# Kernel optimization log

Hardware: AMD Instinct MI355X
Metric: run time of the kernel (lower is better)

The kernel has to match this reference:

```python
import jax, jax.numpy as jnp
import numpy as np

B, T = 4, 16000
V = 256      # input_channels (token vocab)
R = 256      # residual_channels
S = 512      # skip_channels
O = 256      # output_channels
L = 16       # layers
DIL = 256    # 2 ** (floor(log2(max_dilation=128)) + 1) -- same for every layer (as in source)


def setup_inputs() -> dict:
    key = jax.random.key(0)
    ks = jax.random.split(key, 12)
    tokens = jax.random.randint(ks[0], (B, T), 0, V)
    embed = jax.random.normal(ks[1], (V, R), jnp.float32) * 0.05
    dilate_w = jax.random.normal(ks[2], (L, 2 * R, R, 2), jnp.float32) * 0.05
    dilate_b = jax.random.normal(ks[3], (L, 2 * R), jnp.float32) * 0.01
    res_w = jax.random.normal(ks[4], (L - 1, R, R), jnp.float32) * 0.05
    res_b = jax.random.normal(ks[5], (L - 1, R), jnp.float32) * 0.01
    skip_w = jax.random.normal(ks[6], (L, S, R), jnp.float32) * 0.05
    skip_b = jax.random.normal(ks[7], (L, S), jnp.float32) * 0.01
    conv_out_w = jax.random.normal(ks[8], (O, S), jnp.float32) * 0.05
    conv_end_w = jax.random.normal(ks[9], (O, O), jnp.float32) * 0.05
    return {
        'tokens': tokens, 'embed': embed,
        'dilate_w': dilate_w, 'dilate_b': dilate_b,
        'res_w': res_w, 'res_b': res_b,
        'skip_w': skip_w, 'skip_b': skip_b,
        'conv_out_w': conv_out_w, 'conv_end_w': conv_end_w,
    }


def _wavenet(tokens, embed, dilate_w, dilate_b, res_w, res_b, skip_w, skip_b,
             conv_out_w, conv_end_w):
    x = embed[tokens]                 # [B,T,R]
    x = jnp.transpose(x, (0, 2, 1))   # [B,R,T]
    skip = None
    for l in range(L):
        # causal dilated conv, kernel=2: y[t] = W0 @ x[t-DIL] + W1 @ x[t] + b
        x_shift = jnp.pad(x, ((0, 0), (0, 0), (DIL, 0)))[:, :, :T]
        in_act = (jnp.einsum('oi,bit->bot', dilate_w[l, :, :, 0], x_shift)
                  + jnp.einsum('oi,bit->bot', dilate_w[l, :, :, 1], x)
                  + dilate_b[l][None, :, None])      # [B,2R,T]
        g = in_act[:, :R, :]                          # source uses SAME slice for tanh & sigmoid
        act = jnp.tanh(g) * jax.nn.sigmoid(g)         # [B,R,T]
        if l < L - 1:
            res = jnp.einsum('oi,bit->bot', res_w[l], act) + res_b[l][None, :, None]
            x = res + x
        s = jnp.einsum('si,bit->bst', skip_w[l], act) + skip_b[l][None, :, None]
        skip = s if skip is None else skip + s
    out = jax.nn.relu(skip)
    out = jnp.einsum('os,bst->bot', conv_out_w, out)
    out = jax.nn.relu(out)
    out = jnp.einsum('po,bot->bpt', conv_end_w, out)
    return jax.nn.softmax(out, axis=1)                # softmax over channel dim


def reference(tokens, embed, dilate_w, dilate_b, res_w, res_b, skip_w, skip_b,
              conv_out_w, conv_end_w):
    return _wavenet(tokens, embed, dilate_w, dilate_b, res_w, res_b,
                    skip_w, skip_b, conv_out_w, conv_end_w)
```

## Files before the change

kernel.cpp:

```cpp
#include <hip/hip_runtime.h>
#include <hip/hip_fp16.h>

#define TLEN 16000
#define BC 2
#define XPROWS 16256

typedef _Float16 h16;
typedef __attribute__((ext_vector_type(8))) _Float16 half8;
typedef __attribute__((ext_vector_type(4))) _Float16 half4;
typedef __attribute__((ext_vector_type(4))) float f32x4;

__device__ __forceinline__ void gload16(const void* g, void* l) {
  __builtin_amdgcn_global_load_lds((const __attribute__((address_space(1))) void*)g,
                                   (__attribute__((address_space(3))) void*)l, 16, 0, 0);
}

__device__ __forceinline__ float gated_act(float g) {
  float gc = fmaxf(g, -30.0f);
  float e1 = __expf(-gc);
  float e2 = e1 * e1;
  return (1.0f - e2) / ((1.0f + e2) * (1.0f + e1));
}

__global__ __launch_bounds__(256) void prep_k(
    const float* __restrict__ dw, const float* __restrict__ rw,
    const float* __restrict__ sw, const float* __restrict__ cow,
    const float* __restrict__ cew, const float* __restrict__ sb,
    h16* __restrict__ w2h, h16* __restrict__ rsw, h16* __restrict__ couth,
    h16* __restrict__ cendh, float* __restrict__ sbias, h16* __restrict__ x16p)
{
  size_t u = (size_t)blockIdx.x * 256 + threadIdx.x;
  if (u < 2097152) {
    int l = (int)(u >> 17);
    int rem = (int)(u & 131071);
    int o = rem >> 9, k = rem & 511;
    float v = (k < 256) ? dw[(((size_t)l * 512 + o) * 256 + k) * 2]
                        : dw[(((size_t)l * 512 + o) * 256 + (k - 256)) * 2 + 1];
    w2h[u] = (h16)v;
    return;
  }
  u -= 2097152;
  if (u < 3145728) {
    int l = (int)(u / 196608);
    int r = (int)(u % 196608);
    int row = r >> 8, c = r & 255;
    float v;
    if (row < 256) v = (l < 15) ? rw[((size_t)l * 256 + row) * 256 + c] : 0.f;
    else           v = sw[((size_t)l * 512 + (row - 256)) * 256 + c];
    rsw[u] = (h16)v;
    return;
  }
  u -= 3145728;
  if (u < 131072) { couth[u] = (h16)cow[u]; return; }
  u -= 131072;
  if (u < 65536) { cendh[u] = (h16)cew[u]; return; }
  u -= 65536;
  if (u < 512) {
    float s = 0.f;
    for (int l = 0; l < 16; l++) s += sb[(size_t)l * 512 + u];
    sbias[u] = s;
    return;
  }
  u -= 512;
  if (u < 131072) {
    int b = (int)(u >> 16), off = (int)(u & 65535);
    x16p[(size_t)b * XPROWS * 256 + off] = (h16)0.f;
  }
}

__global__ __launch_bounds__(256) void embed_k(
    const int* __restrict__ tok, const float* __restrict__ emb,
    float* __restrict__ x, h16* __restrict__ x16p)
{
  const int b = blockIdx.y;
  const size_t i = (size_t)blockIdx.x * 256 + threadIdx.x;
  const int t = (int)(i >> 6);
  const int c4 = (int)(i & 63) * 4;
  const int tk = tok[(size_t)b * TLEN + t];
  f32x4 v = *(const f32x4*)(emb + (size_t)tk * 256 + c4);
  *(f32x4*)(x + ((size_t)b * TLEN + t) * 256 + c4) = v;
  half4 hv;
#pragma unroll
  for (int j = 0; j < 4; j++) hv[j] = (h16)v[j];
  *(half4*)(x16p + (size_t)b * XPROWS * 256 + (size_t)(t + 256) * 256 + c4) = hv;
}

__global__ __launch_bounds__(256) void skipinit_k(
    const float* __restrict__ sbias, float* __restrict__ skip)
{
  const int b = blockIdx.y;
  const size_t i = (size_t)blockIdx.x * 256 + threadIdx.x;
  const int t = (int)(i >> 7);
  const int s4 = (int)(i & 127) * 4;
  *(f32x4*)(skip + ((size_t)b * TLEN + t) * 512 + s4) = *(const f32x4*)(sbias + s4);
}

__global__ __launch_bounds__(256) void cvt_k(
    const float* __restrict__ skip, h16* __restrict__ sk16)
{
  const size_t i = ((size_t)blockIdx.y * 8192000) + ((size_t)blockIdx.x * 256 + threadIdx.x) * 4;
  f32x4 v = *(const f32x4*)(skip + i);
  half4 hv;
#pragma unroll
  for (int j = 0; j < 4; j++) hv[j] = (h16)fmaxf(v[j], 0.f);
  *(half4*)(sk16 + i) = hv;
}

template<int KTOT, int MODE>
__global__ __launch_bounds__(256) void gemm3_k(
    const h16* __restrict__ A, const h16* __restrict__ W,
    const float* __restrict__ bias, h16* __restrict__ o16,
    float* __restrict__ of32, float* __restrict__ ofskip, int nskip0)
{
  constexpr int NT = KTOT / 32;
  __shared__ h16 As[2][64 * 32];
  __shared__ h16 Bs[2][256 * 32];
  __shared__ h16 tbuf[4][16][72];

  const int tid  = threadIdx.x;
  const int lane = tid & 63;
  const int w    = tid >> 6;
  const int r16  = lane & 15;
  const int kg   = lane >> 4;
  const int t0   = blockIdx.x * 64;
  const int by   = blockIdx.y;
  const int bz   = blockIdx.z;
  const int srow  = lane >> 2;
  const int sunit = (lane & 3) * 8;

  const h16* Ab;
  if constexpr (MODE == 0)      Ab = A + (size_t)bz * XPROWS * 256;
  else if constexpr (MODE == 1) Ab = A + (size_t)bz * TLEN * 256;
  else                          Ab = A + (size_t)bz * TLEN * 512;
  const int n0w = (MODE == 1) ? by * 256 : 0;

  auto stage = [&](int bi, int kk) {
    const int k0 = kk * 32;
    {
      const h16* src;
      if constexpr (MODE == 0)
        src = Ab + (size_t)(t0 + w * 16 + srow + (k0 < 256 ? 0 : 256)) * 256 + (k0 & 255) + sunit;
      else if constexpr (MODE == 1)
        src = Ab + (size_t)(t0 + w * 16 + srow) * 256 + k0 + sunit;
      else
        src = Ab + (size_t)(t0 + w * 16 + srow) * 512 + k0 + sunit;
      gload16(src, &As[bi][(w * 16) * 32]);
    }
#pragma unroll
    for (int q = 0; q < 4; q++) {
      const h16* src = W + (size_t)(n0w + w * 64 + q * 16 + srow) * KTOT + k0 + sunit;
      gload16(src, &Bs[bi][(w * 64 + q * 16) * 32]);
    }
  };

  f32x4 acc[4][4];
#pragma unroll
  for (int i = 0; i < 4; i++)
#pragma unroll
    for (int j = 0; j < 4; j++) acc[i][j] = (f32x4){0.f, 0.f, 0.f, 0.f};

  stage(0, 0);
  __syncthreads();

  for (int t = 0; t < NT; t++) {
    const int cur = t & 1;
    if (t + 1 < NT) stage(cur ^ 1, t + 1);
    half8 af[4], bf[4];
#pragma unroll
    for (int mi = 0; mi < 4; mi++)
      af[mi] = *(const half8*)&As[cur][(mi * 16 + r16) * 32 + kg * 8];
#pragma unroll
    for (int ni = 0; ni < 4; ni++)
      bf[ni] = *(const half8*)&Bs[cur][(w * 64 + ni * 16 + r16) * 32 + kg * 8];
#pragma unroll
    for (int mi = 0; mi < 4; mi++)
#pragma unroll
      for (int ni = 0; ni < 4; ni++)
        acc[mi][ni] = __builtin_amdgcn_mfma_f32_16x16x32_f16(af[mi], bf[ni], acc[mi][ni], 0, 0, 0);
    __syncthreads();
  }

  const int rr = lane >> 2;
  const int cc = (lane & 3) * 16;
  const bool is_res = (MODE == 1) && (n0w < nskip0);

  if constexpr (MODE == 1) {
    if (!is_res) {
#pragma unroll
      for (int mi = 0; mi < 4; mi++)
#pragma unroll
        for (int ni = 0; ni < 4; ni++) {
          const int s = n0w + w * 64 + ni * 16 + r16 - nskip0;
#pragma unroll
          for (int g = 0; g < 4; g++) {
            const int t = t0 + mi * 16 + kg * 4 + g;
            const size_t ix = ((size_t)bz * TLEN + t) * 512 + s;
            ofskip[ix] += acc[mi][ni][g];
          }
        }
      return;
    }
  }

#pragma unroll
  for (int mi = 0; mi < 4; mi++) {
#pragma unroll
    for (int ni = 0; ni < 4; ni++) {
      const int nl = w * 64 + ni * 16 + r16;
#pragma unroll
      for (int g = 0; g < 4; g++) {
        float v = acc[mi][ni][g];
        const int t = t0 + mi * 16 + kg * 4 + g;
        if constexpr (MODE == 0) {
          v = gated_act(v + bias[nl]);
        } else if constexpr (MODE == 1) {
          const size_t ix = ((size_t)bz * TLEN + t) * 256 + nl;
          v = of32[ix] + v + bias[nl];
          of32[ix] = v;
        } else {
          v = fmaxf(v, 0.f);
        }
        tbuf[w][kg * 4 + g][ni * 16 + r16] = (h16)v;
      }
    }
    h16* dst;
    if constexpr (MODE == 1)
      dst = o16 + (size_t)bz * XPROWS * 256 + (size_t)(256 + t0 + mi * 16 + rr) * 256 + w * 64 + cc;
    else
      dst = o16 + ((size_t)bz * TLEN + t0 + mi * 16 + rr) * 256 + w * 64 + cc;
    *(half8*)dst       = *(const half8*)&tbuf[w][rr][cc];
    *(half8*)(dst + 8) = *(const half8*)&tbuf[w][rr][cc + 8];
  }
}

__global__ __launch_bounds__(256) void head_k(
    const h16* __restrict__ A, const h16* __restrict__ W, float* __restrict__ out)
{
  __shared__ h16 As[32][40];
  __shared__ h16 Bs[256][40];
  __shared__ float lg[32][257];

  const int tid = threadIdx.x;
  const int bz  = blockIdx.z;
  const int t0  = blockIdx.x * 32;
  const int lane = tid & 63, wid = tid >> 6;
  const int r16 = lane & 15, kg = lane >> 4;
  const h16* Ab = A + (size_t)bz * TLEN * 256;

  f32x4 acc[2][4];
#pragma unroll
  for (int i = 0; i < 2; i++)
#pragma unroll
    for (int j = 0; j < 4; j++) acc[i][j] = (f32x4){0.f, 0.f, 0.f, 0.f};

  const int arow = tid >> 3, asub = tid & 7;

  for (int k0 = 0; k0 < 256; k0 += 32) {
    {
      const h16* src = Ab + (size_t)(t0 + arow) * 256 + k0 + asub * 4;
      *(half4*)&As[arow][asub * 4] = *(const half4*)src;
    }
    {
      const h16* src = W + (size_t)tid * 256 + k0;
#pragma unroll
      for (int q = 0; q < 4; q++) *(half8*)&Bs[tid][q * 8] = *(const half8*)(src + q * 8);
    }
    __syncthreads();
    half8 af[2], bf[4];
#pragma unroll
    for (int mi = 0; mi < 2; mi++) af[mi] = *(const half8*)&As[mi * 16 + r16][kg * 8];
#pragma unroll
    for (int ni = 0; ni < 4; ni++) bf[ni] = *(const half8*)&Bs[wid * 64 + ni * 16 + r16][kg * 8];
#pragma unroll
    for (int mi = 0; mi < 2; mi++)
#pragma unroll
      for (int ni = 0; ni < 4; ni++)
        acc[mi][ni] = __builtin_amdgcn_mfma_f32_16x16x32_f16(af[mi], bf[ni], acc[mi][ni], 0, 0, 0);
    __syncthreads();
  }

#pragma unroll
  for (int mi = 0; mi < 2; mi++) {
    const int rl = mi * 16 + kg * 4;
#pragma unroll
    for (int ni = 0; ni < 4; ni++) {
      const int n = wid * 64 + ni * 16 + r16;
#pragma unroll
      for (int g = 0; g < 4; g++) lg[rl + g][n] = acc[mi][ni][g];
    }
  }
  __syncthreads();

  for (int i = 0; i < 8; i++) {
    const int r = wid * 8 + i;
    float v[4];
#pragma unroll
    for (int j = 0; j < 4; j++) v[j] = lg[r][lane + 64 * j];
    float m = fmaxf(fmaxf(v[0], v[1]), fmaxf(v[2], v[3]));
#pragma unroll
    for (int off = 32; off >= 1; off >>= 1) m = fmaxf(m, __shfl_xor(m, off));
    float s = 0.f;
#pragma unroll
    for (int j = 0; j < 4; j++) { v[j] = __expf(v[j] - m); s += v[j]; }
#pragma unroll
    for (int off = 32; off >= 1; off >>= 1) s += __shfl_xor(s, off);
    const float inv = 1.f / s;
#pragma unroll
    for (int j = 0; j < 4; j++) lg[r][lane + 64 * j] = v[j] * inv;
  }
  __syncthreads();

  const int tl = tid & 31, og = tid >> 5;
  for (int j = 0; j < 32; j++) {
    const int o = og * 32 + j;
    out[((size_t)bz * 256 + o) * TLEN + t0 + tl] = lg[tl][o];
  }
}

extern "C" void kernel_launch(void* const* d_in, const int* in_sizes, int n_in,
                              void* d_out, int out_size, void* d_ws, size_t ws_size,
                              hipStream_t stream)
{
  const int*   tokens = (const int*)  d_in[0];
  const float* embedw = (const float*)d_in[1];
  const float* dil_w  = (const float*)d_in[2];
  const float* dil_b  = (const float*)d_in[3];
  const float* resw   = (const float*)d_in[4];
  const float* resb   = (const float*)d_in[5];
  const float* skipw  = (const float*)d_in[6];
  const float* skipb  = (const float*)d_in[7];
  const float* coutw  = (const float*)d_in[8];
  const float* cendw  = (const float*)d_in[9];
  float* out = (float*)d_out;

  char* p = (char*)d_ws;
  auto carve = [&](size_t bytes) { char* r = p; p += (bytes + 255) & ~(size_t)255; return r; };
  h16* w2h      = (h16*)carve((size_t)16 * 256 * 512 * 2);
  h16* rsw      = (h16*)carve((size_t)16 * 768 * 256 * 2);
  h16* couth    = (h16*)carve((size_t)256 * 512 * 2);
  h16* cendh    = (h16*)carve((size_t)256 * 256 * 2);
  float* sbias  = (float*)carve(512 * 4);
  float* xf32   = (float*)carve((size_t)BC * TLEN * 256 * 4);
  h16*  x16p    = (h16*) carve((size_t)BC * XPROWS * 256 * 2);
  h16*  act     = (h16*) carve((size_t)BC * TLEN * 256 * 2);
  float* skipf  = (float*)carve((size_t)BC * TLEN * 512 * 4);
  h16* sk16 = (h16*)xf32;
  h16* h116 = act;

  prep_k<<<dim3(21762), 256, 0, stream>>>(
      dil_w, resw, skipw, coutw, cendw, skipb, w2h, rsw, couth, cendh, sbias, x16p);

  for (int c0 = 0; c0 < 4; c0 += BC) {
    const int* tk = tokens + (size_t)c0 * TLEN;

    embed_k<<<dim3(4000, BC), 256, 0, stream>>>(tk, embedw, xf32, x16p);
    skipinit_k<<<dim3(8000, BC), 256, 0, stream>>>(sbias, skipf);

    for (int l = 0; l < 16; l++) {
      gemm3_k<512, 0><<<dim3(250, 1, BC), 256, 0, stream>>>(
          x16p, w2h + (size_t)l * 131072, dil_b + (size_t)l * 512,
          act, nullptr, nullptr, 0);
      if (l < 15)
        gemm3_k<256, 1><<<dim3(250, 3, BC), 256, 0, stream>>>(
            act, rsw + (size_t)l * 196608, resb + (size_t)l * 256,
            x16p, xf32, skipf, 256);
      else
        gemm3_k<256, 1><<<dim3(250, 2, BC), 256, 0, stream>>>(
            act, rsw + (size_t)15 * 196608 + 65536, nullptr,
            x16p, xf32, skipf, 0);
    }

    cvt_k<<<dim3(8000, BC), 256, 0, stream>>>(skipf, sk16);
    gemm3_k<512, 2><<<dim3(250, 1, BC), 256, 0, stream>>>(
        sk16, couth, nullptr, h116, nullptr, nullptr, 0);
    head_k<<<dim3(500, 1, BC), 256, 0, stream>>>(h116, cendh, out + (size_t)c0 * 256 * TLEN);
  }
}
```

Baseline: 2.472 ms.

## Batch skip convolutions into two large-K GEMMs over stored activations

Instead of accumulating each layer's skip projection into an fp32 skip buffer with read-modify-write, the per-layer gated activations are kept in a wide [T,2048] buffer (8 layers at a time). The skip sum is then computed as two K=2048 GEMMs whose epilogue fuses the bias, ReLU and fp16 conversion, which removes the skipinit and cvt kernels. The residual GEMM now updates x with vectorised loads and stores through shared memory, uses a 128-wide N tile, and runs one batch element per pass instead of two. This trades per-layer skip RMW traffic for a larger activation buffer and a smaller grid per launch.

After: 2.714 ms. +9.8%, slower.

```diff
diff --git a/kernel.cpp b/kernel.cpp
--- a/kernel.cpp
+++ b/kernel.cpp
@@ -2,8 +2,6 @@
 #include <hip/hip_fp16.h>
 
 #define TLEN 16000
-#define BC 2
-#define XPROWS 16256
 
 typedef _Float16 h16;
 typedef __attribute__((ext_vector_type(8))) _Float16 half8;
@@ -26,8 +24,9 @@
     const float* __restrict__ dw, const float* __restrict__ rw,
     const float* __restrict__ sw, const float* __restrict__ cow,
     const float* __restrict__ cew, const float* __restrict__ sb,
-    h16* __restrict__ w2h, h16* __restrict__ rsw, h16* __restrict__ couth,
-    h16* __restrict__ cendh, float* __restrict__ sbias, h16* __restrict__ x16p)
+    h16* __restrict__ w2h, h16* __restrict__ resh, h16* __restrict__ skiph,
+    h16* __restrict__ couth, h16* __restrict__ cendh, float* __restrict__ sbias,
+    h16* __restrict__ x16p)
 {
   size_t u = (size_t)blockIdx.x * 256 + threadIdx.x;
   if (u < 2097152) {
@@ -40,17 +39,16 @@
     return;
   }
   u -= 2097152;
-  if (u < 3145728) {
-    int l = (int)(u / 196608);
-    int r = (int)(u % 196608);
-    int row = r >> 8, c = r & 255;
-    float v;
-    if (row < 256) v = (l < 15) ? rw[((size_t)l * 256 + row) * 256 + c] : 0.f;
-    else           v = sw[((size_t)l * 512 + (row - 256)) * 256 + c];
-    rsw[u] = (h16)v;
+  if (u < 983040) { resh[u] = (h16)rw[u]; return; }
+  u -= 983040;
+  if (u < 2097152) {
+    int s = (int)(u >> 12);
+    int r = (int)(u & 4095);
+    int l = r >> 8, c = r & 255;
+    skiph[u] = (h16)sw[((size_t)l * 512 + s) * 256 + c];
     return;
   }
-  u -= 3145728;
+  u -= 2097152;
   if (u < 131072) { couth[u] = (h16)cow[u]; return; }
   u -= 131072;
   if (u < 65536) { cendh[u] = (h16)cew[u]; return; }
@@ -62,60 +60,39 @@
     return;
   }
   u -= 512;
-  if (u < 131072) {
-    int b = (int)(u >> 16), off = (int)(u & 65535);
-    x16p[(size_t)b * XPROWS * 256 + off] = (h16)0.f;
-  }
+  if (u < 65536) x16p[u] = (h16)0.f;
 }
 
 __global__ __launch_bounds__(256) void embed_k(
     const int* __restrict__ tok, const float* __restrict__ emb,
     float* __restrict__ x, h16* __restrict__ x16p)
 {
-  const int b = blockIdx.y;
   const size_t i = (size_t)blockIdx.x * 256 + threadIdx.x;
   const int t = (int)(i >> 6);
   const int c4 = (int)(i & 63) * 4;
-  const int tk = tok[(size_t)b * TLEN + t];
+  const int tk = tok[t];
   f32x4 v = *(const f32x4*)(emb + (size_t)tk * 256 + c4);
-  *(f32x4*)(x + ((size_t)b * TLEN + t) * 256 + c4) = v;
+  *(f32x4*)(x + (size_t)t * 256 + c4) = v;
   half4 hv;
 #pragma unroll
   for (int j = 0; j < 4; j++) hv[j] = (h16)v[j];
-  *(half4*)(x16p + (size_t)b * XPROWS * 256 + (size_t)(t + 256) * 256 + c4) = hv;
-}
-
-__global__ __launch_bounds__(256) void skipinit_k(
-    const float* __restrict__ sbias, float* __restrict__ skip)
-{
-  const int b = blockIdx.y;
-  const size_t i = (size_t)blockIdx.x * 256 + threadIdx.x;
-  const int t = (int)(i >> 7);
-  const int s4 = (int)(i & 127) * 4;
-  *(f32x4*)(skip + ((size_t)b * TLEN + t) * 512 + s4) = *(const f32x4*)(sbias + s4);
-}
-
-__global__ __launch_bounds__(256) void cvt_k(
-    const float* __restrict__ skip, h16* __restrict__ sk16)
-{
-  const size_t i = ((size_t)blockIdx.y * 8192000) + ((size_t)blockIdx.x * 256 + threadIdx.x) * 4;
-  f32x4 v = *(const f32x4*)(skip + i);
-  half4 hv;
-#pragma unroll
-  for (int j = 0; j < 4; j++) hv[j] = (h16)fmaxf(v[j], 0.f);
-  *(half4*)(sk16 + i) = hv;
-}
-
-template<int KTOT, int MODE>
-__global__ __launch_bounds__(256) void gemm3_k(
+  *(half4*)(x16p + (size_t)(t + 256) * 256 + c4) = hv;
+}
+
+template<int KTOT, int AST, int WST, int BN, int MODE>
+__global__ __launch_bounds__(256) void gemm4_k(
     const h16* __restrict__ A, const h16* __restrict__ W,
     const float* __restrict__ bias, h16* __restrict__ o16,
-    float* __restrict__ of32, float* __restrict__ ofskip, int nskip0)
+    float* __restrict__ of32, const float* __restrict__ sp_in)
 {
   constexpr int NT = KTOT / 32;
+  constexpr int MI = (BN == 128) ? 2 : 4;
+  constexpr int OST = (MODE == 0) ? 2048 : (MODE == 3) ? 512 : 256;
   __shared__ h16 As[2][64 * 32];
-  __shared__ h16 Bs[2][256 * 32];
-  __shared__ h16 tbuf[4][16][72];
+  __shared__ h16 Bs[2][BN * 32];
+  __shared__ __align__(16) char tscr[17408];
+  h16 (*tbufH)[16][72] = (h16(*)[16][72])tscr;
+  float (*tbufF)[16][68] = (float(*)[16][68])tscr;
 
   const int tid  = threadIdx.x;
   const int lane = tid & 63;
@@ -123,39 +100,35 @@
   const int r16  = lane & 15;
   const int kg   = lane >> 4;
   const int t0   = blockIdx.x * 64;
-  const int by   = blockIdx.y;
-  const int bz   = blockIdx.z;
+  const int n0w  = blockIdx.y * BN;
+  const int wm   = (BN == 128) ? (w >> 1) : 0;
+  const int wn   = (BN == 128) ? (w & 1) : w;
+  const int arow_base = wm * 32;
+  const int brow_base = wn * 64;
   const int srow  = lane >> 2;
   const int sunit = (lane & 3) * 8;
-
-  const h16* Ab;
-  if constexpr (MODE == 0)      Ab = A + (size_t)bz * XPROWS * 256;
-  else if constexpr (MODE == 1) Ab = A + (size_t)bz * TLEN * 256;
-  else                          Ab = A + (size_t)bz * TLEN * 512;
-  const int n0w = (MODE == 1) ? by * 256 : 0;
 
   auto stage = [&](int bi, int kk) {
     const int k0 = kk * 32;
     {
       const h16* src;
       if constexpr (MODE == 0)
-        src = Ab + (size_t)(t0 + w * 16 + srow + (k0 < 256 ? 0 : 256)) * 256 + (k0 & 255) + sunit;
-      else if constexpr (MODE == 1)
-        src = Ab + (size_t)(t0 + w * 16 + srow) * 256 + k0 + sunit;
+        src = A + (size_t)(t0 + w * 16 + srow + (k0 < 256 ? 0 : 256)) * AST + (k0 & 255) + sunit;
       else
-        src = Ab + (size_t)(t0 + w * 16 + srow) * 512 + k0 + sunit;
+        src = A + (size_t)(t0 + w * 16 + srow) * AST + k0 + sunit;
       gload16(src, &As[bi][(w * 16) * 32]);
     }
 #pragma unroll
-    for (int q = 0; q < 4; q++) {
-      const h16* src = W + (size_t)(n0w + w * 64 + q * 16 + srow) * KTOT + k0 + sunit;
-      gload16(src, &Bs[bi][(w * 64 + q * 16) * 32]);
+    for (int q = 0; q < BN / 64; q++) {
+      const int row = w * (BN / 4) + q * 16;
+      const h16* src = W + (size_t)(n0w + row + srow) * WST + k0 + sunit;
+      gload16(src, &Bs[bi][row * 32]);
     }
   };
 
-  f32x4 acc[4][4];
-#pragma unroll
-  for (int i = 0; i < 4; i++)
+  f32x4 acc[MI][4];
+#pragma unroll
+  for (int i = 0; i < MI; i++)
 #pragma unroll
     for (int j = 0; j < 4; j++) acc[i][j] = (f32x4){0.f, 0.f, 0.f, 0.f};
 
@@ -165,15 +138,15 @@
   for (int t = 0; t < NT; t++) {
     const int cur = t & 1;
     if (t + 1 < NT) stage(cur ^ 1, t + 1);
-    half8 af[4], bf[4];
-#pragma unroll
-    for (int mi = 0; mi < 4; mi++)
-      af[mi] = *(const half8*)&As[cur][(mi * 16 + r16) * 32 + kg * 8];
+    half8 af[MI], bf[4];
+#pragma unroll
+    for (int mi = 0; mi < MI; mi++)
+      af[mi] = *(const half8*)&As[cur][(arow_base + mi * 16 + r16) * 32 + kg * 8];
 #pragma unroll
     for (int ni = 0; ni < 4; ni++)
-      bf[ni] = *(const half8*)&Bs[cur][(w * 64 + ni * 16 + r16) * 32 + kg * 8];
-#pragma unroll
-    for (int mi = 0; mi < 4; mi++)
+      bf[ni] = *(const half8*)&Bs[cur][(brow_base + ni * 16 + r16) * 32 + kg * 8];
+#pragma unroll
+    for (int mi = 0; mi < MI; mi++)
 #pragma unroll
       for (int ni = 0; ni < 4; ni++)
         acc[mi][ni] = __builtin_amdgcn_mfma_f32_16x16x32_f16(af[mi], bf[ni], acc[mi][ni], 0, 0, 0);
@@ -182,54 +155,77 @@
 
   const int rr = lane >> 2;
   const int cc = (lane & 3) * 16;
-  const bool is_res = (MODE == 1) && (n0w < nskip0);
-
-  if constexpr (MODE == 1) {
-    if (!is_res) {
-#pragma unroll
-      for (int mi = 0; mi < 4; mi++)
-#pragma unroll
-        for (int ni = 0; ni < 4; ni++) {
-          const int s = n0w + w * 64 + ni * 16 + r16 - nskip0;
-#pragma unroll
-          for (int g = 0; g < 4; g++) {
-            const int t = t0 + mi * 16 + kg * 4 + g;
-            const size_t ix = ((size_t)bz * TLEN + t) * 512 + s;
-            ofskip[ix] += acc[mi][ni][g];
+  const int colw = n0w + brow_base;
+
+#pragma unroll
+  for (int mi = 0; mi < MI; mi++) {
+    const int trow = t0 + arow_base + mi * 16;
+    if constexpr (MODE == 1 || MODE == 2 || MODE == 3) {
+#pragma unroll
+      for (int ni = 0; ni < 4; ni++)
+#pragma unroll
+        for (int g = 0; g < 4; g++) {
+          float v = acc[mi][ni][g];
+          if constexpr (MODE == 1) v += bias[colw + ni * 16 + r16];
+          tbufF[w][kg * 4 + g][ni * 16 + r16] = v;
+        }
+      if constexpr (MODE == 1) {
+        float* xrow = of32 + (size_t)(trow + rr) * 256 + colw + cc;
+        h16* xprow = o16 + (size_t)(trow + rr + 256) * 256 + colw + cc;
+        half8 hv0, hv1;
+#pragma unroll
+        for (int j = 0; j < 4; j++) {
+          f32x4 v = *(const f32x4*)(xrow + j * 4);
+          f32x4 d = *(const f32x4*)&tbufF[w][rr][cc + j * 4];
+          v += d;
+          *(f32x4*)(xrow + j * 4) = v;
+#pragma unroll
+          for (int e = 0; e < 4; e++) {
+            if (j < 2) hv0[j * 4 + e] = (h16)v[e];
+            else       hv1[(j - 2) * 4 + e] = (h16)v[e];
           }
         }
-      return;
-    }
-  }
-
-#pragma unroll
-  for (int mi = 0; mi < 4; mi++) {
-#pragma unroll
-    for (int ni = 0; ni < 4; ni++) {
-      const int nl = w * 64 + ni * 16 + r16;
-#pragma unroll
-      for (int g = 0; g < 4; g++) {
-        float v = acc[mi][ni][g];
-        const int t = t0 + mi * 16 + kg * 4 + g;
-        if constexpr (MODE == 0) {
-          v = gated_act(v + bias[nl]);
-        } else if constexpr (MODE == 1) {
-          const size_t ix = ((size_t)bz * TLEN + t) * 256 + nl;
-          v = of32[ix] + v + bias[nl];
-          of32[ix] = v;
-        } else {
-          v = fmaxf(v, 0.f);
+        *(half8*)xprow       = hv0;
+        *(half8*)(xprow + 8) = hv1;
+      } else if constexpr (MODE == 2) {
+        float* dst = of32 + (size_t)(trow + rr) * 512 + colw + cc;
+#pragma unroll
+        for (int j = 0; j < 4; j++)
+          *(f32x4*)(dst + j * 4) = *(const f32x4*)&tbufF[w][rr][cc + j * 4];
+      } else {
+        const float* sprow = sp_in + (size_t)(trow + rr) * 512 + colw + cc;
+        h16* dst = o16 + (size_t)(trow + rr) * 512 + colw + cc;
+        half8 hv0, hv1;
+#pragma unroll
+        for (int j = 0; j < 4; j++) {
+          f32x4 v = *(const f32x4*)&tbufF[w][rr][cc + j * 4];
+          f32x4 s = *(const f32x4*)(sprow + j * 4);
+          f32x4 sb = *(const f32x4*)(bias + colw + cc + j * 4);
+          v = v + s + sb;
+#pragma unroll
+          for (int e = 0; e < 4; e++) {
+            float r = fmaxf(v[e], 0.f);
+            if (j < 2) hv0[j * 4 + e] = (h16)r;
+            else       hv1[(j - 2) * 4 + e] = (h16)r;
+          }
         }
-        tbuf[w][kg * 4 + g][ni * 16 + r16] = (h16)v;
+        *(half8*)dst       = hv0;
+        *(half8*)(dst + 8) = hv1;
       }
-    }
-    h16* dst;
-    if constexpr (MODE == 1)
-      dst = o16 + (size_t)bz * XPROWS * 256 + (size_t)(256 + t0 + mi * 16 + rr) * 256 + w * 64 + cc;
-    else
-      dst = o16 + ((size_t)bz * TLEN + t0 + mi * 16 + rr) * 256 + w * 64 + cc;
-    *(half8*)dst       = *(const half8*)&tbuf[w][rr][cc];
-    *(half8*)(dst + 8) = *(const half8*)&tbuf[w][rr][cc + 8];
+    } else {
+#pragma unroll
+      for (int ni = 0; ni < 4; ni++)
+#pragma unroll
+        for (int g = 0; g < 4; g++) {
+          float v = acc[mi][ni][g];
+          if constexpr (MODE == 0) v = gated_act(v + bias[colw + ni * 16 + r16]);
+          else                     v = fmaxf(v, 0.f);
+          tbufH[w][kg * 4 + g][ni * 16 + r16] = (h16)v;
+        }
+      h16* dst = o16 + (size_t)(trow + rr) * OST + colw + cc;
+      *(half8*)dst       = *(const half8*)&tbufH[w][rr][cc];
+      *(half8*)(dst + 8) = *(const half8*)&tbufH[w][rr][cc + 8];
+    }
   }
 }
 
@@ -241,11 +237,9 @@
   __shared__ float lg[32][257];
 
   const int tid = threadIdx.x;
-  const int bz  = blockIdx.z;
   const int t0  = blockIdx.x * 32;
   const int lane = tid & 63, wid = tid >> 6;
   const int r16 = lane & 15, kg = lane >> 4;
-  const h16* Ab = A + (size_t)bz * TLEN * 256;
 
   f32x4 acc[2][4];
 #pragma unroll
@@ -257,7 +251,7 @@
 
   for (int k0 = 0; k0 < 256; k0 += 32) {
     {
-      const h16* src = Ab + (size_t)(t0 + arow) * 256 + k0 + asub * 4;
+      const h16* src = A + (size_t)(t0 + arow) * 256 + k0 + asub * 4;
       *(half4*)&As[arow][asub * 4] = *(const half4*)src;
     }
     {
@@ -313,7 +307,7 @@
   const int tl = tid & 31, og = tid >> 5;
   for (int j = 0; j < 32; j++) {
     const int o = og * 32 + j;
-    out[((size_t)bz * 256 + o) * TLEN + t0 + tl] = lg[tl][o];
+    out[(size_t)o * TLEN + t0 + tl] = lg[tl][o];
   }
 }
 
@@ -336,43 +330,42 @@
   char* p = (char*)d_ws;
   auto carve = [&](size_t bytes) { char* r = p; p += (bytes + 255) & ~(size_t)255; return r; };
   h16* w2h      = (h16*)carve((size_t)16 * 256 * 512 * 2);
-  h16* rsw      = (h16*)carve((size_t)16 * 768 * 256 * 2);
+  h16* resh     = (h16*)carve((size_t)15 * 256 * 256 * 2);
+  h16* skiph    = (h16*)carve((size_t)512 * 4096 * 2);
   h16* couth    = (h16*)carve((size_t)256 * 512 * 2);
   h16* cendh    = (h16*)carve((size_t)256 * 256 * 2);
   float* sbias  = (float*)carve(512 * 4);
-  float* xf32   = (float*)carve((size_t)BC * TLEN * 256 * 4);
-  h16*  x16p    = (h16*) carve((size_t)BC * XPROWS * 256 * 2);
-  h16*  act     = (h16*) carve((size_t)BC * TLEN * 256 * 2);
-  float* skipf  = (float*)carve((size_t)BC * TLEN * 512 * 4);
+  float* xf32   = (float*)carve((size_t)TLEN * 256 * 4);
+  h16*  x16p    = (h16*) carve((size_t)(TLEN + 256) * 256 * 2);
+  h16*  act     = (h16*) carve((size_t)TLEN * 2048 * 2);
+  float* sp     = (float*)carve((size_t)TLEN * 512 * 4);
   h16* sk16 = (h16*)xf32;
   h16* h116 = act;
 
-  prep_k<<<dim3(21762), 256, 0, stream>>>(
-      dil_w, resw, skipw, coutw, cendw, skipb, w2h, rsw, couth, cendh, sbias, x16p);
-
-  for (int c0 = 0; c0 < 4; c0 += BC) {
-    const int* tk = tokens + (size_t)c0 * TLEN;
-
-    embed_k<<<dim3(4000, BC), 256, 0, stream>>>(tk, embedw, xf32, x16p);
-    skipinit_k<<<dim3(8000, BC), 256, 0, stream>>>(sbias, skipf);
+  prep_k<<<dim3(21250), 256, 0, stream>>>(
+      dil_w, resw, skipw, coutw, cendw, skipb,
+      w2h, resh, skiph, couth, cendh, sbias, x16p);
+
+  for (int b = 0; b < 4; b++) {
+    embed_k<<<dim3(4000), 256, 0, stream>>>(tokens + (size_t)b * TLEN, embedw, xf32, x16p);
 
     for (int l = 0; l < 16; l++) {
-      gemm3_k<512, 0><<<dim3(250, 1, BC), 256, 0, stream>>>(
+      gemm4_k<512, 256, 512, 128, 0><<<dim3(250, 2), 256, 0, stream>>>(
           x16p, w2h + (size_t)l * 131072, dil_b + (size_t)l * 512,
-          act, nullptr, nullptr, 0);
+          act + (l & 7) * 256, nullptr, nullptr);
       if (l < 15)
-        gemm3_k<256, 1><<<dim3(250, 3, BC), 256, 0, stream>>>(
-            act, rsw + (size_t)l * 196608, resb + (size_t)l * 256,
-            x16p, xf32, skipf, 256);
-      else
-        gemm3_k<256, 1><<<dim3(250, 2, BC), 256, 0, stream>>>(
-            act, rsw + (size_t)15 * 196608 + 65536, nullptr,
-            x16p, xf32, skipf, 0);
-    }
-
-    cvt_k<<<dim3(8000, BC), 256, 0, stream>>>(skipf, sk16);
-    gemm3_k<512, 2><<<dim3(250, 1, BC), 256, 0, stream>>>(
-        sk16, couth, nullptr, h116, nullptr, nullptr, 0);
-    head_k<<<dim3(500, 1, BC), 256, 0, stream>>>(h116, cendh, out + (size_t)c0 * 256 * TLEN);
-  }
-}
+        gemm4_k<256, 2048, 256, 128, 1><<<dim3(250, 2), 256, 0, stream>>>(
+            act + (l & 7) * 256, resh + (size_t)l * 65536, resb + (size_t)l * 256,
+            x16p, xf32, nullptr);
+      if (l == 7)
+        gemm4_k<2048, 2048, 4096, 256, 2><<<dim3(250, 2), 256, 0, stream>>>(
+            act, skiph, nullptr, nullptr, sp, nullptr);
+    }
+
+    gemm4_k<2048, 2048, 4096, 256, 3><<<dim3(250, 2), 256, 0, stream>>>(
+        act, skiph + 2048, sbias, sk16, nullptr, sp);
+    gemm4_k<512, 512, 512, 128, 4><<<dim3(250, 2), 256, 0, stream>>>(
+        sk16, couth, nullptr, h116, nullptr, nullptr);
+    head_k<<<dim3(500), 256, 0, stream>>>(h116, cendh, out + (size_t)b * 256 * TLEN);
+  }
+}
```
